# Kernel tuning notes

Measured on AMD Instinct MI355X. Metric: run time of the kernel, lower is better.

## Reference

```python
import jax, jax.numpy as jnp
import numpy as np

H = 128   # hidden_dim
L = 3     # num_layers
N = 50000
E = 800000
EPS = 1e-5


def setup_inputs() -> dict:
    key = jax.random.key(0)
    ks = jax.random.split(key, 16)
    s = 0.02  # param init scale
    return {
        "edge_index_new": jax.random.randint(ks[0], (2, E), 0, N),
        "aligned_features": jax.random.normal(ks[1], (E, 8), jnp.float32),
        "h_nodes_old": jax.random.normal(ks[2], (N, H), jnp.float32),
        "num_nodes": N,
        # node_fusion: Linear(2H -> H)
        "Wf": jax.random.normal(ks[3], (2 * H, H), jnp.float32) * s,
        "bf": jnp.zeros((H,), jnp.float32),
        # edge_to_weight: Linear(8->H), Linear(H->1)
        "We1": jax.random.normal(ks[4], (8, H), jnp.float32) * s,
        "be1": jnp.zeros((H,), jnp.float32),
        "We2": jax.random.normal(ks[5], (H, 1), jnp.float32) * s,
        "be2": jnp.zeros((1,), jnp.float32),
        # GraphConv per layer: lin_rel (W+b), lin_root (W, no bias)
        "Wrel": jax.random.normal(ks[6], (L, H, H), jnp.float32) * s,
        "brel": jnp.zeros((L, H), jnp.float32),
        "Wroot": jax.random.normal(ks[7], (L, H, H), jnp.float32) * s,
        # LayerNorm per layer
        "gamma": jnp.ones((L, H), jnp.float32),
        "beta": jnp.zeros((L, H), jnp.float32),
        # edge_decoder: Linear(2H+8 -> H), Linear(H -> 1)
        "Wd1": jax.random.normal(ks[8], (2 * H + 8, H), jnp.float32) * s,
        "bd1": jnp.zeros((H,), jnp.float32),
        "Wd2": jax.random.normal(ks[9], (H, 1), jnp.float32) * s,
        "bd2": jnp.zeros((1,), jnp.float32),
    }


def _layer_norm(x, g, b):
    mu = jnp.mean(x, axis=-1, keepdims=True)
    var = jnp.mean((x - mu) ** 2, axis=-1, keepdims=True)
    return (x - mu) * jax.lax.rsqrt(var + EPS) * g + b


def reference(edge_index_new, aligned_features, h_nodes_old, num_nodes,
              Wf, bf, We1, be1, We2, be2,
              Wrel, brel, Wroot, gamma, beta,
              Wd1, bd1, Wd2, bd2):
    dt = h_nodes_old.dtype
    hd = Wf.shape[1]
    # node_fusion(cat([ones, h_old])) ; dropout is identity in eval
    x_init = jnp.ones((num_nodes, hd), dtype=dt)
    x = jax.nn.relu(jnp.concatenate([x_init, h_nodes_old], axis=-1) @ Wf + bf)
    # edge_to_weight -> scalar per edge
    ew = jax.nn.sigmoid(jax.nn.relu(aligned_features @ We1 + be1) @ We2 + be2)[:, 0]
    src, dst = edge_index_new[0], edge_index_new[1]
    n_layers = Wrel.shape[0]
    for l in range(n_layers):
        x_res = x
        # GraphConv: sum_{j->i} w_e * x[j], then lin_rel(agg) + lin_root(x)
        msg = ew[:, None] * x[src]                         # [E, H]
        agg = jax.ops.segment_sum(msg, dst, num_segments=num_nodes)
        h = agg @ Wrel[l] + brel[l] + x @ Wroot[l]
        h = jax.nn.relu(_layer_norm(h, gamma[l], beta[l]))
        x = h + x_res
    # edge decoder on gathered node pairs + raw 8-dim features
    edge_repr = jnp.concatenate([x[src], x[dst], aligned_features], axis=-1)
    hmid = jax.nn.relu(edge_repr @ Wd1 + bd1)
    return hmid @ Wd2 + bd2
```

## Files before the change

kernel.cpp:

```cpp
#include <hip/hip_runtime.h>
#include <hip/hip_bf16.h>

#define H 128
#define LN_EPS 1e-5f

typedef __attribute__((ext_vector_type(8))) short bf16x8;
typedef __attribute__((ext_vector_type(4))) float f32x4;

static __device__ __forceinline__ unsigned short f2bf(float f) {
  unsigned u = __float_as_uint(f);
  unsigned r = (u + 0x7fff + ((u >> 16) & 1)) >> 16;
  return (unsigned short)r;
}
static __device__ __forceinline__ float bf2f(unsigned short s) {
  return __uint_as_float(((unsigned)s) << 16);
}


__global__ void zero_int_kernel(int* __restrict__ p, int n) {
  int i = blockIdx.x * blockDim.x + threadIdx.x;
  if (i < n) p[i] = 0;
}

__global__ __launch_bounds__(1024) void prep_cvec_kernel(const float* __restrict__ Wf,
                                                         const float* __restrict__ bf,
                                                         float* __restrict__ cvec) {
  __shared__ float part[8][128];
  int tid = threadIdx.x;
  int col = tid & 127, seg = tid >> 7;
  float s = 0.f;
  for (int r = seg * 16; r < seg * 16 + 16; ++r) s += Wf[r * H + col];
  part[seg][col] = s;
  __syncthreads();
  if (tid < 128) {
    float t = bf[tid];
#pragma unroll
    for (int g = 0; g < 8; ++g) t += part[g][tid];
    cvec[tid] = t;
  }
}

__global__ void count_kernel(const int* __restrict__ ei, int E, int* __restrict__ cnt) {
  int e = blockIdx.x * blockDim.x + threadIdx.x;
  if (e < E) atomicAdd(&cnt[ei[E + e]], 1);
}

__global__ __launch_bounds__(1024) void scan_kernel(const int* __restrict__ cnt,
                                                    int* __restrict__ off,
                                                    int* __restrict__ pos, int N) {
  __shared__ int wtot[16];
  __shared__ int wbase[16];
  __shared__ int s_btot;
  __shared__ int s_carry;
  int tid = threadIdx.x, lane = tid & 63, wid = tid >> 6;
  if (tid == 0) s_carry = 0;
  __syncthreads();
  for (int base = 0; base < N; base += 4096) {
    int i0 = base + tid * 4;
    int v[4];
#pragma unroll
    for (int j = 0; j < 4; ++j) v[j] = (i0 + j < N) ? cnt[i0 + j] : 0;
    int s = v[0] + v[1] + v[2] + v[3];
    int incl = s;
#pragma unroll
    for (int o = 1; o < 64; o <<= 1) {
      int t = __shfl_up(incl, o, 64);
      if (lane >= o) incl += t;
    }
    if (lane == 63) wtot[wid] = incl;
    __syncthreads();
    if (tid == 0) {
      int run = 0;
      for (int w = 0; w < 16; ++w) { wbase[w] = run; run += wtot[w]; }
      s_btot = run;
    }
    __syncthreads();
    int e0 = s_carry + wbase[wid] + (incl - s);
#pragma unroll
    for (int j = 0; j < 4; ++j) {
      if (i0 + j < N) { off[i0 + j] = e0; pos[i0 + j] = e0; }
      e0 += v[j];
    }
    __syncthreads();
    if (tid == 0) s_carry += s_btot;
    __syncthreads();
  }
  if (tid == 0) off[N] = s_carry;
}

__global__ void fill_kernel(const int* __restrict__ ei, const float* __restrict__ ew, int E,
                            int* __restrict__ pos, uint2* __restrict__ csr) {
  int e = blockIdx.x * blockDim.x + threadIdx.x;
  if (e < E) {
    int d = ei[E + e];
    int p = atomicAdd(&pos[d], 1);
    csr[p] = make_uint2((unsigned)ei[e], __float_as_uint(ew[e]));
  }
}

__global__ __launch_bounds__(256) void pack_w_kernel(const float* __restrict__ Wf,
                                                     const float* __restrict__ Wrel,
                                                     const float* __restrict__ Wroot,
                                                     const float* __restrict__ Wd1,
                                                     unsigned short* __restrict__ wpk) {
  int id = blockIdx.x * blockDim.x + threadIdx.x;
  if (id >= 9 * 2048) return;
  int l = id & 63, nf = (id >> 6) & 7, kk = (id >> 9) & 3, m = id >> 11;
  const float* src;
  if (m == 0) src = Wf + H * H;
  else if (m <= 3) src = Wrel + (size_t)(m - 1) * H * H;
  else if (m <= 6) src = Wroot + (size_t)(m - 4) * H * H;
  else src = Wd1 + (size_t)(m - 7) * H * H;
  int col = nf * 16 + (l & 15);
  int kbase = kk * 32 + (l >> 4) * 8;
  unsigned short t[8];
#pragma unroll
  for (int j = 0; j < 8; ++j) t[j] = f2bf(src[(size_t)(kbase + j) * H + col]);
  *(uint4*)&wpk[(size_t)id * 8] = *(uint4*)t;
}

__global__ __launch_bounds__(256) void edge_weight_v3_kernel(
    const float* __restrict__ af, const float* __restrict__ We1, const float* __restrict__ be1,
    const float* __restrict__ We2, const float* __restrict__ be2, float* __restrict__ ew, int E) {
  int lane = threadIdx.x & 63;
  int sub = lane & 15;
  int grp = lane >> 4;
  float w1[8][8], b1[8], w2[8];
#pragma unroll
  for (int i = 0; i < 8; ++i)
#pragma unroll
    for (int c = 0; c < 8; ++c) w1[i][c] = We1[i * H + sub * 8 + c];
#pragma unroll
  for (int c = 0; c < 8; ++c) { b1[c] = be1[sub * 8 + c]; w2[c] = We2[sub * 8 + c]; }
  float b2 = be2[0];
  int gw = (blockIdx.x * blockDim.x + threadIdx.x) >> 6;
  int nw = (gridDim.x * blockDim.x) >> 6;
  int n4 = (E + 3) >> 2;
  for (int e4 = gw; e4 < n4; e4 += nw) {
    int e = e4 * 4 + grp;
    bool valid = e < E;
    int ee = valid ? e : E - 1;
    float4 a0 = *(const float4*)&af[(size_t)ee * 8];
    float4 a1 = *(const float4*)&af[(size_t)ee * 8 + 4];
    float afv[8] = {a0.x, a0.y, a0.z, a0.w, a1.x, a1.y, a1.z, a1.w};
    float t[8];
#pragma unroll
    for (int c = 0; c < 8; ++c) t[c] = b1[c];
#pragma unroll
    for (int i = 0; i < 8; ++i)
#pragma unroll
      for (int c = 0; c < 8; ++c) t[c] += afv[i] * w1[i][c];
    float p = 0.f;
#pragma unroll
    for (int c = 0; c < 8; ++c) p += fmaxf(t[c], 0.f) * w2[c];
    p += __shfl_xor(p, 1, 64);
    p += __shfl_xor(p, 2, 64);
    p += __shfl_xor(p, 4, 64);
    p += __shfl_xor(p, 8, 64);
    if (valid && sub == 0) {
      float s = p + b2;
      ew[e] = 1.f / (1.f + expf(-s));
    }
  }
}

__global__ __launch_bounds__(256) void gemm_init_kernel(
    const float* __restrict__ Xf, const unsigned short* __restrict__ Wp,
    const float* __restrict__ bias, unsigned short* __restrict__ Y, int M) {
  int l = threadIdx.x & 63, w = threadIdx.x >> 6;
  int lr = l & 15, lg = l >> 4;
  int m0 = blockIdx.x * 128 + w * 32;
  f32x4 acc[2][8] = {};
  for (int kk = 0; kk < 4; ++kk) {
    bf16x8 a[2];
#pragma unroll
    for (int mi = 0; mi < 2; ++mi) {
      int row = m0 + mi * 16 + lr;
      if (row >= M) row = M - 1;
      const float* xp = &Xf[(size_t)row * H + kk * 32 + lg * 8];
      float4 u0 = *(const float4*)xp;
      float4 u1 = *(const float4*)(xp + 4);
      unsigned short t[8] = {f2bf(u0.x), f2bf(u0.y), f2bf(u0.z), f2bf(u0.w),
                             f2bf(u1.x), f2bf(u1.y), f2bf(u1.z), f2bf(u1.w)};
      a[mi] = *(const bf16x8*)t;
    }
#pragma unroll
    for (int nf = 0; nf < 8; ++nf) {
      bf16x8 b = *(const bf16x8*)&Wp[(size_t)(kk * 8 + nf) * 512 + l * 8];
#pragma unroll
      for (int mi = 0; mi < 2; ++mi)
        acc[mi][nf] = __builtin_amdgcn_mfma_f32_16x16x32_bf16(a[mi], b, acc[mi][nf], 0, 0, 0);
    }
  }
  float bv[8];
#pragma unroll
  for (int nf = 0; nf < 8; ++nf) bv[nf] = bias[nf * 16 + lr];
#pragma unroll
  for (int mi = 0; mi < 2; ++mi)
#pragma unroll
    for (int r = 0; r < 4; ++r) {
      int row = m0 + mi * 16 + lg * 4 + r;
      if (row < M) {
#pragma unroll
        for (int nf = 0; nf < 8; ++nf)
          Y[(size_t)row * H + nf * 16 + lr] = f2bf(fmaxf(acc[mi][nf][r] + bv[nf], 0.f));
      }
    }
}

__global__ __launch_bounds__(256) void gemm_layer_ln_kernel(
    const unsigned short* __restrict__ Agg, const unsigned short* __restrict__ WpRel,
    unsigned short* __restrict__ Xio, const unsigned short* __restrict__ WpRoot,
    const float* __restrict__ brel, const float* __restrict__ gamma,
    const float* __restrict__ beta, int M) {
  int l = threadIdx.x & 63, w = threadIdx.x >> 6;
  int lr = l & 15, lg = l >> 4;
  int m0 = blockIdx.x * 128 + w * 32;
  f32x4 acc[2][8] = {};
  for (int kk = 0; kk < 8; ++kk) {
    const unsigned short* X = (kk >= 4) ? Xio : Agg;
    const unsigned short* Wp = (kk >= 4) ? WpRoot : WpRel;
    int k4 = kk & 3;
    bf16x8 a[2] = {};
#pragma unroll
    for (int mi = 0; mi < 2; ++mi) {
      int row = m0 + mi * 16 + lr;
      if (row < M) a[mi] = *(const bf16x8*)&X[(size_t)row * H + k4 * 32 + lg * 8];
    }
#pragma unroll
    for (int nf = 0; nf < 8; ++nf) {
      bf16x8 b = *(const bf16x8*)&Wp[(size_t)(k4 * 8 + nf) * 512 + l * 8];
#pragma unroll
      for (int mi = 0; mi < 2; ++mi)
        acc[mi][nf] = __builtin_amdgcn_mfma_f32_16x16x32_bf16(a[mi], b, acc[mi][nf], 0, 0, 0);
    }
  }
  float bv[8], gv[8], bev[8];
#pragma unroll
  for (int nf = 0; nf < 8; ++nf) {
    int col = nf * 16 + lr;
    bv[nf] = brel[col]; gv[nf] = gamma[col]; bev[nf] = beta[col];
  }
#pragma unroll
  for (int mi = 0; mi < 2; ++mi) {
#pragma unroll
    for (int r = 0; r < 4; ++r) {
      int row = m0 + mi * 16 + lg * 4 + r;
      float hv[8], s1 = 0.f;
#pragma unroll
      for (int nf = 0; nf < 8; ++nf) { hv[nf] = acc[mi][nf][r] + bv[nf]; s1 += hv[nf]; }
      s1 += __shfl_xor(s1, 1, 64);
      s1 += __shfl_xor(s1, 2, 64);
      s1 += __shfl_xor(s1, 4, 64);
      s1 += __shfl_xor(s1, 8, 64);
      float mu = s1 * (1.0f / H);
      float s2 = 0.f;
#pragma unroll
      for (int nf = 0; nf < 8; ++nf) { float d = hv[nf] - mu; s2 += d * d; }
      s2 += __shfl_xor(s2, 1, 64);
      s2 += __shfl_xor(s2, 2, 64);
      s2 += __shfl_xor(s2, 4, 64);
      s2 += __shfl_xor(s2, 8, 64);
      float rstd = rsqrtf(s2 * (1.0f / H) + LN_EPS);
      if (row < M) {
#pragma unroll
        for (int nf = 0; nf < 8; ++nf) {
          int col = nf * 16 + lr;
          float v = fmaxf((hv[nf] - mu) * rstd * gv[nf] + bev[nf], 0.f);
          v += bf2f(Xio[(size_t)row * H + col]);
          Xio[(size_t)row * H + col] = f2bf(v);
        }
      }
    }
  }
}

__global__ __launch_bounds__(256) void gemm_dec_kernel(
    const unsigned short* __restrict__ X, const unsigned short* __restrict__ WpA,
    const unsigned short* __restrict__ WpB, const float* __restrict__ bd1,
    unsigned short* __restrict__ Aout, unsigned short* __restrict__ Bout, int M) {
  int l = threadIdx.x & 63, w = threadIdx.x >> 6;
  int lr = l & 15, lg = l >> 4;
  int m0 = blockIdx.x * 128 + w * 32;
  f32x4 accA[2][8] = {};
  f32x4 accB[2][8] = {};
  for (int kk = 0; kk < 4; ++kk) {
    bf16x8 a[2];
#pragma unroll
    for (int mi = 0; mi < 2; ++mi) {
      int row = m0 + mi * 16 + lr;
      if (row >= M) row = M - 1;
      a[mi] = *(const bf16x8*)&X[(size_t)row * H + kk * 32 + lg * 8];
    }
#pragma unroll
    for (int nf = 0; nf < 8; ++nf) {
      bf16x8 bA = *(const bf16x8*)&WpA[(size_t)(kk * 8 + nf) * 512 + l * 8];
      bf16x8 bB = *(const bf16x8*)&WpB[(size_t)(kk * 8 + nf) * 512 + l * 8];
#pragma unroll
      for (int mi = 0; mi < 2; ++mi) {
        accA[mi][nf] = __builtin_amdgcn_mfma_f32_16x16x32_bf16(a[mi], bA, accA[mi][nf], 0, 0, 0);
        accB[mi][nf] = __builtin_amdgcn_mfma_f32_16x16x32_bf16(a[mi], bB, accB[mi][nf], 0, 0, 0);
      }
    }
  }
  float bdv[8];
#pragma unroll
  for (int nf = 0; nf < 8; ++nf) bdv[nf] = bd1[nf * 16 + lr];
#pragma unroll
  for (int mi = 0; mi < 2; ++mi)
#pragma unroll
    for (int r = 0; r < 4; ++r) {
      int row = m0 + mi * 16 + lg * 4 + r;
      if (row < M) {
#pragma unroll
        for (int nf = 0; nf < 8; ++nf) {
          int col = nf * 16 + lr;
          Aout[(size_t)row * H + col] = f2bf(accA[mi][nf][r] + bdv[nf]);
          Bout[(size_t)row * H + col] = f2bf(accB[mi][nf][r]);
        }
      }
    }
}

__global__ __launch_bounds__(256) void gather_agg_v2_kernel(
    const unsigned short* __restrict__ xbf, const int* __restrict__ off,
    const uint2* __restrict__ csr, unsigned short* __restrict__ aggbf, int N) {
  int gw = (blockIdx.x * blockDim.x + threadIdx.x) >> 6;
  int lane = threadIdx.x & 63;
  int nw = (gridDim.x * blockDim.x) >> 6;
  for (int n = gw; n < N; n += nw) {
    int s0 = off[n], s1 = off[n + 1];
    float ax = 0.f, ay = 0.f;
    for (int base = s0; base < s1; base += 8) {
      unsigned srcv[8];
      float wv[8];
#pragma unroll
      for (int j = 0; j < 8; ++j) {
        int id = base + j;
        int cid = id < s1 ? id : s1 - 1;
        uint2 c = csr[cid];
        srcv[j] = c.x;
        wv[j] = (id < s1) ? __uint_as_float(c.y) : 0.f;
      }
      unsigned vv[8];
#pragma unroll
      for (int j = 0; j < 8; ++j)
        vv[j] = *(const unsigned*)&xbf[(size_t)srcv[j] * H + lane * 2];
#pragma unroll
      for (int j = 0; j < 8; ++j) {
        ax += wv[j] * bf2f((unsigned short)(vv[j] & 0xffffu));
        ay += wv[j] * bf2f((unsigned short)(vv[j] >> 16));
      }
    }
    unsigned o = (unsigned)f2bf(ax) | ((unsigned)f2bf(ay) << 16);
    *(unsigned*)&aggbf[(size_t)n * H + lane * 2] = o;
  }
}

__global__ __launch_bounds__(256) void edge_out_v3_kernel(
    const int* __restrict__ ei, const float* __restrict__ af,
    const unsigned short* __restrict__ A, const unsigned short* __restrict__ B,
    const float* __restrict__ Wd1c, const float* __restrict__ Wd2,
    const float* __restrict__ bd2, float* __restrict__ out, int E) {
  int lane = threadIdx.x & 63;
  int sub = lane & 15;
  int grp = lane >> 4;
  float wc[8][8], w2[8];
#pragma unroll
  for (int i = 0; i < 8; ++i)
#pragma unroll
    for (int c = 0; c < 8; ++c) wc[i][c] = Wd1c[i * H + sub * 8 + c];
#pragma unroll
  for (int c = 0; c < 8; ++c) w2[c] = Wd2[sub * 8 + c];
  float b2 = bd2[0];
  int gw = (blockIdx.x * blockDim.x + threadIdx.x) >> 6;
  int nw = (gridDim.x * blockDim.x) >> 6;
  int n4 = (E + 3) >> 2;
  for (int e4 = gw; e4 < n4; e4 += nw) {
    int e = e4 * 4 + grp;
    bool valid = e < E;
    int ee = valid ? e : E - 1;
    int s = ei[ee], d = ei[E + ee];
    uint4 va = *(const uint4*)&A[(size_t)s * H + sub * 8];
    uint4 vb = *(const uint4*)&B[(size_t)d * H + sub * 8];
    float4 a0 = *(const float4*)&af[(size_t)ee * 8];
    float4 a1 = *(const float4*)&af[(size_t)ee * 8 + 4];
    float afv[8] = {a0.x, a0.y, a0.z, a0.w, a1.x, a1.y, a1.z, a1.w};
    const unsigned* pa = (const unsigned*)&va;
    const unsigned* pb = (const unsigned*)&vb;
    float t[8];
#pragma unroll
    for (int q = 0; q < 4; ++q) {
      unsigned av = pa[q], bv = pb[q];
      t[q * 2 + 0] = bf2f((unsigned short)(av & 0xffffu)) + bf2f((unsigned short)(bv & 0xffffu));
      t[q * 2 + 1] = bf2f((unsigned short)(av >> 16)) + bf2f((unsigned short)(bv >> 16));
    }
#pragma unroll
    for (int i = 0; i < 8; ++i)
#pragma unroll
      for (int c = 0; c < 8; ++c) t[c] += afv[i] * wc[i][c];
    float p = 0.f;
#pragma unroll
    for (int c = 0; c < 8; ++c) p += fmaxf(t[c], 0.f) * w2[c];
    p += __shfl_xor(p, 1, 64);
    p += __shfl_xor(p, 2, 64);
    p += __shfl_xor(p, 4, 64);
    p += __shfl_xor(p, 8, 64);
    if (valid && sub == 0) out[e] = p + b2;
  }
}

extern "C" void kernel_launch(void* const* d_in, const int* in_sizes, int n_in, void* d_out,
                              int out_size, void* d_ws, size_t ws_size, hipStream_t stream) {
  const int* ei = (const int*)d_in[0];
  const float* af = (const float*)d_in[1];
  const float* h_old = (const float*)d_in[2];
  const float* Wf = (const float*)d_in[4];
  const float* bf = (const float*)d_in[5];
  const float* We1 = (const float*)d_in[6];
  const float* be1 = (const float*)d_in[7];
  const float* We2 = (const float*)d_in[8];
  const float* be2 = (const float*)d_in[9];
  const float* Wrel = (const float*)d_in[10];
  const float* brel = (const float*)d_in[11];
  const float* Wroot = (const float*)d_in[12];
  const float* gamma = (const float*)d_in[13];
  const float* beta = (const float*)d_in[14];
  const float* Wd1 = (const float*)d_in[15];
  const float* bd1 = (const float*)d_in[16];
  const float* Wd2 = (const float*)d_in[17];
  const float* bd2 = (const float*)d_in[18];
  const int N = in_sizes[2] / H;
  const int E = in_sizes[1] / 8;
  float* out = (float*)d_out;

  char* p = (char*)d_ws;
  auto alloc = [&](size_t b) { char* r = p; p += (b + 255) & ~(size_t)255; return r; };
  int* cnt = (int*)alloc((size_t)N * 4);
  int* pos = (int*)alloc((size_t)N * 4);
  int* off = (int*)alloc((size_t)(N + 1) * 4);
  uint2* csr = (uint2*)alloc((size_t)E * 8);
  float* ew = (float*)alloc((size_t)E * 4);
  float* cvec = (float*)alloc(H * 4);
  unsigned short* wpk = (unsigned short*)alloc((size_t)9 * 16384 * 2);
  unsigned short* xbf = (unsigned short*)alloc((size_t)N * H * 2);
  unsigned short* aggbf = (unsigned short*)alloc((size_t)N * H * 2);
  unsigned short* buf2 = (unsigned short*)alloc((size_t)N * H * 2);

  unsigned short* Abf = aggbf;
  unsigned short* Bbf = buf2;

  hipLaunchKernelGGL(zero_int_kernel, dim3((N + 255) / 256), dim3(256), 0, stream, cnt, N);
  hipLaunchKernelGGL(prep_cvec_kernel, dim3(1), dim3(1024), 0, stream, Wf, bf, cvec);
  hipLaunchKernelGGL(count_kernel, dim3((E + 255) / 256), dim3(256), 0, stream, ei, E, cnt);
  hipLaunchKernelGGL(scan_kernel, dim3(1), dim3(1024), 0, stream, cnt, off, pos, N);
  hipLaunchKernelGGL(edge_weight_v3_kernel, dim3(4096), dim3(256), 0, stream, af, We1, be1,
                     We2, be2, ew, E);
  hipLaunchKernelGGL(fill_kernel, dim3((E + 255) / 256), dim3(256), 0, stream, ei, ew, E, pos,
                     csr);
  hipLaunchKernelGGL(pack_w_kernel, dim3(72), dim3(256), 0, stream, Wf, Wrel, Wroot, Wd1, wpk);

  int gblocks = (N + 127) / 128;
  hipLaunchKernelGGL(gemm_init_kernel, dim3(gblocks), dim3(256), 0, stream, h_old, wpk, cvec,
                     xbf, N);

  for (int l = 0; l < 3; ++l) {
    hipLaunchKernelGGL(gather_agg_v2_kernel, dim3((N + 3) / 4), dim3(256), 0, stream, xbf, off,
                       csr, aggbf, N);
    hipLaunchKernelGGL(gemm_layer_ln_kernel, dim3(gblocks), dim3(256), 0, stream, aggbf,
                       wpk + (size_t)(1 + l) * 16384, xbf, wpk + (size_t)(4 + l) * 16384,
                       brel + l * H, gamma + l * H, beta + l * H, N);
  }

  hipLaunchKernelGGL(gemm_dec_kernel, dim3(gblocks), dim3(256), 0, stream, xbf,
                     wpk + (size_t)7 * 16384, wpk + (size_t)8 * 16384, bd1, Abf, Bbf, N);
  hipLaunchKernelGGL(edge_out_v3_kernel, dim3(4096), dim3(256), 0, stream, ei, af, Abf, Bbf,
                     Wd1 + 2 * H * H, Wd2, bd2, out, E);
}
```

Baseline: 466.1 us.

## Fuse edge MLP into CSR fill, widen gather, decode edges per destination node

The edge-weight MLP now does the CSR fill in the same pass, and it also writes each edge's id and its 8 raw features in CSR order. This removes a separate kernel and the ew round-trip through memory. The gather kernel handles two nodes per wavefront, with 4 features per lane and 16 edges in flight. The edge decoder walks edges grouped by destination node, so B[dst] is loaded once per node and A[src] plus the features are prefetched. In exchange there are extra writes for af_csr and eid, the decoder's output writes are scattered, and per-node loop lengths are uneven, which can cause load imbalance.

```diff
diff --git a/kernel.cpp b/kernel.cpp
--- a/kernel.cpp
+++ b/kernel.cpp
@@ -86,16 +86,6 @@
     __syncthreads();
   }
   if (tid == 0) off[N] = s_carry;
-}
-
-__global__ void fill_kernel(const int* __restrict__ ei, const float* __restrict__ ew, int E,
-                            int* __restrict__ pos, uint2* __restrict__ csr) {
-  int e = blockIdx.x * blockDim.x + threadIdx.x;
-  if (e < E) {
-    int d = ei[E + e];
-    int p = atomicAdd(&pos[d], 1);
-    csr[p] = make_uint2((unsigned)ei[e], __float_as_uint(ew[e]));
-  }
 }
 
 __global__ __launch_bounds__(256) void pack_w_kernel(const float* __restrict__ Wf,
@@ -119,9 +109,11 @@
   *(uint4*)&wpk[(size_t)id * 8] = *(uint4*)t;
 }
 
-__global__ __launch_bounds__(256) void edge_weight_v3_kernel(
-    const float* __restrict__ af, const float* __restrict__ We1, const float* __restrict__ be1,
-    const float* __restrict__ We2, const float* __restrict__ be2, float* __restrict__ ew, int E) {
+__global__ __launch_bounds__(256) void edge_mlp_fill_kernel(
+    const int* __restrict__ ei, const float* __restrict__ af, const float* __restrict__ We1,
+    const float* __restrict__ be1, const float* __restrict__ We2, const float* __restrict__ be2,
+    int* __restrict__ pos, uint2* __restrict__ csr, int* __restrict__ csr_eid,
+    float* __restrict__ af_csr, int E) {
   int lane = threadIdx.x & 63;
   int sub = lane & 15;
   int grp = lane >> 4;
@@ -157,10 +149,16 @@
     p += __shfl_xor(p, 2, 64);
     p += __shfl_xor(p, 4, 64);
     p += __shfl_xor(p, 8, 64);
+    int ppos = 0;
     if (valid && sub == 0) {
-      float s = p + b2;
-      ew[e] = 1.f / (1.f + expf(-s));
-    }
+      float w = 1.f / (1.f + expf(-(p + b2)));
+      int d = ei[E + e];
+      ppos = atomicAdd(&pos[d], 1);
+      csr[ppos] = make_uint2((unsigned)ei[e], __float_as_uint(w));
+      csr_eid[ppos] = e;
+    }
+    ppos = __shfl(ppos, grp * 16, 64);
+    if (valid && sub < 8) af_csr[(size_t)ppos * 8 + sub] = afv[sub];
   }
 }
 
@@ -322,46 +320,49 @@
     }
 }
 
-__global__ __launch_bounds__(256) void gather_agg_v2_kernel(
+__global__ __launch_bounds__(256) void gather_agg_v3_kernel(
     const unsigned short* __restrict__ xbf, const int* __restrict__ off,
     const uint2* __restrict__ csr, unsigned short* __restrict__ aggbf, int N) {
   int gw = (blockIdx.x * blockDim.x + threadIdx.x) >> 6;
   int lane = threadIdx.x & 63;
-  int nw = (gridDim.x * blockDim.x) >> 6;
-  for (int n = gw; n < N; n += nw) {
+  int half = lane >> 5, li = lane & 31;
+  int n = gw * 2 + half;
+  if (n < N) {
     int s0 = off[n], s1 = off[n + 1];
-    float ax = 0.f, ay = 0.f;
-    for (int base = s0; base < s1; base += 8) {
-      unsigned srcv[8];
-      float wv[8];
-#pragma unroll
-      for (int j = 0; j < 8; ++j) {
+    float a0 = 0.f, a1 = 0.f, a2 = 0.f, a3 = 0.f;
+    for (int base = s0; base < s1; base += 16) {
+      uint2 c[16];
+#pragma unroll
+      for (int j = 0; j < 16; ++j) {
         int id = base + j;
-        int cid = id < s1 ? id : s1 - 1;
-        uint2 c = csr[cid];
-        srcv[j] = c.x;
-        wv[j] = (id < s1) ? __uint_as_float(c.y) : 0.f;
-      }
-      unsigned vv[8];
-#pragma unroll
-      for (int j = 0; j < 8; ++j)
-        vv[j] = *(const unsigned*)&xbf[(size_t)srcv[j] * H + lane * 2];
-#pragma unroll
-      for (int j = 0; j < 8; ++j) {
-        ax += wv[j] * bf2f((unsigned short)(vv[j] & 0xffffu));
-        ay += wv[j] * bf2f((unsigned short)(vv[j] >> 16));
-      }
-    }
-    unsigned o = (unsigned)f2bf(ax) | ((unsigned)f2bf(ay) << 16);
-    *(unsigned*)&aggbf[(size_t)n * H + lane * 2] = o;
-  }
-}
-
-__global__ __launch_bounds__(256) void edge_out_v3_kernel(
-    const int* __restrict__ ei, const float* __restrict__ af,
-    const unsigned short* __restrict__ A, const unsigned short* __restrict__ B,
-    const float* __restrict__ Wd1c, const float* __restrict__ Wd2,
-    const float* __restrict__ bd2, float* __restrict__ out, int E) {
+        c[j] = csr[id < s1 ? id : s1 - 1];
+        if (id >= s1) c[j].y = 0;
+      }
+      uint2 v[16];
+#pragma unroll
+      for (int j = 0; j < 16; ++j)
+        v[j] = *(const uint2*)&xbf[(size_t)c[j].x * H + li * 4];
+#pragma unroll
+      for (int j = 0; j < 16; ++j) {
+        float w = __uint_as_float(c[j].y);
+        a0 += w * bf2f((unsigned short)(v[j].x & 0xffffu));
+        a1 += w * bf2f((unsigned short)(v[j].x >> 16));
+        a2 += w * bf2f((unsigned short)(v[j].y & 0xffffu));
+        a3 += w * bf2f((unsigned short)(v[j].y >> 16));
+      }
+    }
+    unsigned o0 = (unsigned)f2bf(a0) | ((unsigned)f2bf(a1) << 16);
+    unsigned o1 = (unsigned)f2bf(a2) | ((unsigned)f2bf(a3) << 16);
+    *(uint2*)&aggbf[(size_t)n * H + li * 4] = make_uint2(o0, o1);
+  }
+}
+
+__global__ __launch_bounds__(256) void edge_out_v4_kernel(
+    const int* __restrict__ off, const uint2* __restrict__ csr, const int* __restrict__ csr_eid,
+    const float* __restrict__ af_csr, const unsigned short* __restrict__ A,
+    const unsigned short* __restrict__ B, const float* __restrict__ Wd1c,
+    const float* __restrict__ Wd2, const float* __restrict__ bd2, float* __restrict__ out,
+    int N) {
   int lane = threadIdx.x & 63;
   int sub = lane & 15;
   int grp = lane >> 4;
@@ -373,40 +374,56 @@
 #pragma unroll
   for (int c = 0; c < 8; ++c) w2[c] = Wd2[sub * 8 + c];
   float b2 = bd2[0];
-  int gw = (blockIdx.x * blockDim.x + threadIdx.x) >> 6;
-  int nw = (gridDim.x * blockDim.x) >> 6;
-  int n4 = (E + 3) >> 2;
-  for (int e4 = gw; e4 < n4; e4 += nw) {
-    int e = e4 * 4 + grp;
-    bool valid = e < E;
-    int ee = valid ? e : E - 1;
-    int s = ei[ee], d = ei[E + ee];
-    uint4 va = *(const uint4*)&A[(size_t)s * H + sub * 8];
-    uint4 vb = *(const uint4*)&B[(size_t)d * H + sub * 8];
-    float4 a0 = *(const float4*)&af[(size_t)ee * 8];
-    float4 a1 = *(const float4*)&af[(size_t)ee * 8 + 4];
-    float afv[8] = {a0.x, a0.y, a0.z, a0.w, a1.x, a1.y, a1.z, a1.w};
-    const unsigned* pa = (const unsigned*)&va;
+  int gg = ((blockIdx.x * blockDim.x + threadIdx.x) >> 6) * 4 + grp;
+  int ng = ((gridDim.x * blockDim.x) >> 6) * 4;
+  for (int n = gg; n < N; n += ng) {
+    int s0 = off[n], s1 = off[n + 1];
+    if (s0 >= s1) continue;
+    uint4 vb = *(const uint4*)&B[(size_t)n * H + sub * 8];
     const unsigned* pb = (const unsigned*)&vb;
-    float t[8];
+    float tb[8];
 #pragma unroll
     for (int q = 0; q < 4; ++q) {
-      unsigned av = pa[q], bv = pb[q];
-      t[q * 2 + 0] = bf2f((unsigned short)(av & 0xffffu)) + bf2f((unsigned short)(bv & 0xffffu));
-      t[q * 2 + 1] = bf2f((unsigned short)(av >> 16)) + bf2f((unsigned short)(bv >> 16));
-    }
-#pragma unroll
-    for (int i = 0; i < 8; ++i)
-#pragma unroll
-      for (int c = 0; c < 8; ++c) t[c] += afv[i] * wc[i][c];
-    float p = 0.f;
-#pragma unroll
-    for (int c = 0; c < 8; ++c) p += fmaxf(t[c], 0.f) * w2[c];
-    p += __shfl_xor(p, 1, 64);
-    p += __shfl_xor(p, 2, 64);
-    p += __shfl_xor(p, 4, 64);
-    p += __shfl_xor(p, 8, 64);
-    if (valid && sub == 0) out[e] = p + b2;
+      tb[q * 2 + 0] = bf2f((unsigned short)(pb[q] & 0xffffu));
+      tb[q * 2 + 1] = bf2f((unsigned short)(pb[q] >> 16));
+    }
+    uint2 c = csr[s0];
+    int eid = csr_eid[s0];
+    uint4 va = *(const uint4*)&A[(size_t)c.x * H + sub * 8];
+    float4 f0 = *(const float4*)&af_csr[(size_t)s0 * 8];
+    float4 f1 = *(const float4*)&af_csr[(size_t)s0 * 8 + 4];
+    for (int k = s0; k < s1; ++k) {
+      uint4 va_c = va;
+      float4 g0 = f0, g1 = f1;
+      int eid_c = eid;
+      if (k + 1 < s1) {
+        c = csr[k + 1];
+        eid = csr_eid[k + 1];
+        va = *(const uint4*)&A[(size_t)c.x * H + sub * 8];
+        f0 = *(const float4*)&af_csr[(size_t)(k + 1) * 8];
+        f1 = *(const float4*)&af_csr[(size_t)(k + 1) * 8 + 4];
+      }
+      const unsigned* pa = (const unsigned*)&va_c;
+      float t[8];
+#pragma unroll
+      for (int q = 0; q < 4; ++q) {
+        t[q * 2 + 0] = tb[q * 2 + 0] + bf2f((unsigned short)(pa[q] & 0xffffu));
+        t[q * 2 + 1] = tb[q * 2 + 1] + bf2f((unsigned short)(pa[q] >> 16));
+      }
+      float afv[8] = {g0.x, g0.y, g0.z, g0.w, g1.x, g1.y, g1.z, g1.w};
+#pragma unroll
+      for (int i = 0; i < 8; ++i)
+#pragma unroll
+        for (int cc = 0; cc < 8; ++cc) t[cc] += afv[i] * wc[i][cc];
+      float p = 0.f;
+#pragma unroll
+      for (int cc = 0; cc < 8; ++cc) p += fmaxf(t[cc], 0.f) * w2[cc];
+      p += __shfl_xor(p, 1, 64);
+      p += __shfl_xor(p, 2, 64);
+      p += __shfl_xor(p, 4, 64);
+      p += __shfl_xor(p, 8, 64);
+      if (sub == 0) out[eid_c] = p + b2;
+    }
   }
 }
 
@@ -440,7 +457,8 @@
   int* pos = (int*)alloc((size_t)N * 4);
   int* off = (int*)alloc((size_t)(N + 1) * 4);
   uint2* csr = (uint2*)alloc((size_t)E * 8);
-  float* ew = (float*)alloc((size_t)E * 4);
+  int* csr_eid = (int*)alloc((size_t)E * 4);
+  float* af_csr = (float*)alloc((size_t)E * 32);
   float* cvec = (float*)alloc(H * 4);
   unsigned short* wpk = (unsigned short*)alloc((size_t)9 * 16384 * 2);
   unsigned short* xbf = (unsigned short*)alloc((size_t)N * H * 2);
@@ -454,18 +472,17 @@
   hipLaunchKernelGGL(prep_cvec_kernel, dim3(1), dim3(1024), 0, stream, Wf, bf, cvec);
   hipLaunchKernelGGL(count_kernel, dim3((E + 255) / 256), dim3(256), 0, stream, ei, E, cnt);
   hipLaunchKernelGGL(scan_kernel, dim3(1), dim3(1024), 0, stream, cnt, off, pos, N);
-  hipLaunchKernelGGL(edge_weight_v3_kernel, dim3(4096), dim3(256), 0, stream, af, We1, be1,
-                     We2, be2, ew, E);
-  hipLaunchKernelGGL(fill_kernel, dim3((E + 255) / 256), dim3(256), 0, stream, ei, ew, E, pos,
-                     csr);
+  hipLaunchKernelGGL(edge_mlp_fill_kernel, dim3(4096), dim3(256), 0, stream, ei, af, We1, be1,
+                     We2, be2, pos, csr, csr_eid, af_csr, E);
   hipLaunchKernelGGL(pack_w_kernel, dim3(72), dim3(256), 0, stream, Wf, Wrel, Wroot, Wd1, wpk);
 
   int gblocks = (N + 127) / 128;
   hipLaunchKernelGGL(gemm_init_kernel, dim3(gblocks), dim3(256), 0, stream, h_old, wpk, cvec,
                      xbf, N);
 
+  int gat_blocks = (N / 2 + 3) / 4;
   for (int l = 0; l < 3; ++l) {
-    hipLaunchKernelGGL(gather_agg_v2_kernel, dim3((N + 3) / 4), dim3(256), 0, stream, xbf, off,
+    hipLaunchKernelGGL(gather_agg_v3_kernel, dim3(gat_blocks), dim3(256), 0, stream, xbf, off,
                        csr, aggbf, N);
     hipLaunchKernelGGL(gemm_layer_ln_kernel, dim3(gblocks), dim3(256), 0, stream, aggbf,
                        wpk + (size_t)(1 + l) * 16384, xbf, wpk + (size_t)(4 + l) * 16384,
@@ -474,6 +491,6 @@
 
   hipLaunchKernelGGL(gemm_dec_kernel, dim3(gblocks), dim3(256), 0, stream, xbf,
                      wpk + (size_t)7 * 16384, wpk + (size_t)8 * 16384, bd1, Abf, Bbf, N);
-  hipLaunchKernelGGL(edge_out_v3_kernel, dim3(4096), dim3(256), 0, stream, ei, af, Abf, Bbf,
-                     Wd1 + 2 * H * H, Wd2, bd2, out, E);
-}
+  hipLaunchKernelGGL(edge_out_v4_kernel, dim3((N + 15) / 16), dim3(256), 0, stream, off, csr,
+                     csr_eid, af_csr, Abf, Bbf, Wd1 + 2 * H * H, Wd2, bd2, out, N);
+}
```

Result: slower. 493.0 us (+5.8%).
